# Kernel optimization log

Hardware: AMD Instinct MI355X
Metric: run time of the kernel (lower is better)

## Reference

```python
import jax, jax.numpy as jnp
import numpy as np

N_TOK, BATCH, D, MEM, H, W = 196, 64, 256, 2048, 16, 16


def setup_inputs() -> dict:
    key = jax.random.key(0)
    ks = jax.random.split(key, 9)
    w_scale = 1.0 / np.sqrt(D)  # ~ Linear default init scale
    return {
        "input_tokens": jax.random.normal(ks[0], (N_TOK, BATCH, D), jnp.float32),
        "ch_memory": jax.random.normal(ks[1], (MEM, D), jnp.float32) * 0.1,
        "ch_wq": jax.random.normal(ks[2], (D, D), jnp.float32) * w_scale,
        "ch_wk": jax.random.normal(ks[3], (D, D), jnp.float32) * w_scale,
        "ch_wv": jax.random.normal(ks[4], (D, D), jnp.float32) * w_scale,
        "sp_memory": jax.random.normal(ks[5], (MEM, H, W), jnp.float32) * 0.1,
        "sp_wq": jax.random.normal(ks[6], (D, D), jnp.float32) * w_scale,
        "sp_wk": jax.random.normal(ks[7], (D, D), jnp.float32) * w_scale,
        "sp_wv": jax.random.normal(ks[8], (D, D), jnp.float32) * w_scale,
    }


def reference(input_tokens, ch_memory, ch_wq, ch_wk, ch_wv,
              sp_memory, sp_wq, sp_wk, sp_wv):
    n_tok, batch, d = input_tokens.shape
    hw = d  # spatial branch requires feature_dim == H*W
    x = input_tokens.reshape(n_tok * batch, d)  # [NB, D]

    # ---- Channel memory branch: dot-product softmax read ----
    q = x @ ch_wq.T                       # [NB, D]
    k = ch_memory @ ch_wk.T               # [M, D]
    v = ch_memory @ ch_wv.T               # [M, D]
    scores = (q @ k.T) * (1.0 / jnp.sqrt(jnp.float32(d)))  # [NB, M]
    att_c = jax.nn.softmax(scores, axis=-1)
    out_c = att_c @ v                     # [NB, D]

    # ---- Spatial memory branch: SSIM-score softmax read ----
    mem_flat = sp_memory.reshape(sp_memory.shape[0], hw)  # [M, HW]
    qf = x @ sp_wq.T                      # [NB, HW]
    kf = mem_flat @ sp_wk.T               # [M, HW]
    vf = mem_flat @ sp_wv.T               # [M, HW]

    q_mean = jnp.mean(qf, axis=1, keepdims=True)          # [NB, 1]
    k_mean = jnp.mean(kf, axis=1, keepdims=True)          # [M, 1]
    q_var = jnp.var(qf, axis=1, ddof=1, keepdims=True)    # unbiased, like torch.var
    k_var = jnp.var(kf, axis=1, ddof=1, keepdims=True)
    cov = ((qf - q_mean) @ (kf - k_mean).T) / jnp.float32(hw - 1)  # [NB, M]

    c1, c2 = 0.01, 0.03
    mean_prod = q_mean @ k_mean.T                          # [NB, M]
    numerator = (2.0 * mean_prod + c1) * (2.0 * cov + c2)
    denominator = (q_mean ** 2 + (k_mean.T) ** 2 + c1) * (q_var + k_var.T + c2)
    ssim = numerator / (denominator + 1e-8)                # [NB, M]

    att_s = jax.nn.softmax(ssim, axis=-1)
    out_s = att_s @ vf                     # [NB, HW] == [NB, D]

    return (out_c + out_s).reshape(n_tok, batch, d)
```

## Files before the change

kernel.cpp:

```cpp
#include <hip/hip_runtime.h>

#define NBQ 12544
#define DM  256
#define MM  2048

typedef __attribute__((ext_vector_type(8)))  __bf16 bf16x8;
typedef __attribute__((ext_vector_type(4)))  float  floatx4;

__device__ __forceinline__ ushort f2bf(float x) {
    unsigned u = __float_as_uint(x);
    u += 0x7fffu + ((u >> 16) & 1u);
    return (ushort)(u >> 16);
}
__device__ __forceinline__ float bf2f(ushort h) {
    return __uint_as_float(((unsigned)h) << 16);
}

__global__ __launch_bounds__(256) void gemm_proj_all(
    const float* __restrict__ x,      const float* __restrict__ ch_mem,
    const float* __restrict__ ch_wq,  const float* __restrict__ ch_wk,
    const float* __restrict__ ch_wv,  const float* __restrict__ sp_mem,
    const float* __restrict__ sp_wq,  const float* __restrict__ sp_wk,
    const float* __restrict__ sp_wv,
    ushort* __restrict__ Qb,  ushort* __restrict__ QFb,
    ushort* __restrict__ Kb,  ushort* __restrict__ KFb,
    ushort* __restrict__ Vtb, ushort* __restrict__ VFtb)
{
    __shared__ ushort As[64][72];
    __shared__ ushort Ws[64][72];

    int bid = blockIdx.x;
    const float* A; const float* W; ushort* C; int nrows, trans;
    if (bid < 1568) {
        if (bid < 784) { A = x; W = ch_wq; C = Qb; }
        else           { A = x; W = sp_wq; C = QFb; bid -= 784; }
        nrows = NBQ; trans = 0;
    } else if (bid < 1824) {
        if (bid < 1696) { A = ch_mem; W = ch_wk; C = Kb;  bid -= 1568; }
        else            { A = sp_mem; W = sp_wk; C = KFb; bid -= 1696; }
        nrows = MM; trans = 0;
    } else {
        if (bid < 1952) { A = ch_mem; W = ch_wv; C = Vtb;  bid -= 1824; }
        else            { A = sp_mem; W = sp_wv; C = VFtb; bid -= 1952; }
        nrows = MM; trans = 1;
    }
    const int r0 = (bid >> 2) * 64;
    const int c0 = (bid & 3) * 64;

    const int tid  = threadIdx.x;
    const int wv   = tid >> 6;
    const int lane = tid & 63;
    const int quad = lane >> 4;
    const int l16  = lane & 15;
    const int rw = (wv & 1) * 32;
    const int cw = (wv >> 1) * 32;

    floatx4 acc[2][2];
    #pragma unroll
    for (int i = 0; i < 2; ++i)
        #pragma unroll
        for (int j = 0; j < 2; ++j)
            acc[i][j] = (floatx4){0.f, 0.f, 0.f, 0.f};

    for (int d0 = 0; d0 < 256; d0 += 64) {
        __syncthreads();
        #pragma unroll
        for (int it = 0; it < 4; ++it) {
            int idx = tid + it * 256;
            int r = idx >> 4, c4 = (idx & 15) * 4;
            float4 a4 = *(const float4*)(A + (size_t)(r0 + r) * 256 + d0 + c4);
            float4 w4 = *(const float4*)(W + (size_t)(c0 + r) * 256 + d0 + c4);
            ushort4 ab, wb;
            ab.x = f2bf(a4.x); ab.y = f2bf(a4.y); ab.z = f2bf(a4.z); ab.w = f2bf(a4.w);
            wb.x = f2bf(w4.x); wb.y = f2bf(w4.y); wb.z = f2bf(w4.z); wb.w = f2bf(w4.w);
            *(ushort4*)&As[r][c4] = ab;
            *(ushort4*)&Ws[r][c4] = wb;
        }
        __syncthreads();
        #pragma unroll
        for (int kk = 0; kk < 64; kk += 32) {
            bf16x8 aA0 = *(const bf16x8*)&As[rw + l16][kk + quad * 8];
            bf16x8 aA1 = *(const bf16x8*)&As[rw + 16 + l16][kk + quad * 8];
            bf16x8 bW0 = *(const bf16x8*)&Ws[cw + l16][kk + quad * 8];
            bf16x8 bW1 = *(const bf16x8*)&Ws[cw + 16 + l16][kk + quad * 8];
            acc[0][0] = __builtin_amdgcn_mfma_f32_16x16x32_bf16(aA0, bW0, acc[0][0], 0, 0, 0);
            acc[0][1] = __builtin_amdgcn_mfma_f32_16x16x32_bf16(aA0, bW1, acc[0][1], 0, 0, 0);
            acc[1][0] = __builtin_amdgcn_mfma_f32_16x16x32_bf16(aA1, bW0, acc[1][0], 0, 0, 0);
            acc[1][1] = __builtin_amdgcn_mfma_f32_16x16x32_bf16(aA1, bW1, acc[1][1], 0, 0, 0);
        }
    }

    if (!trans) {
        #pragma unroll
        for (int ag = 0; ag < 2; ++ag)
            #pragma unroll
            for (int cg = 0; cg < 2; ++cg)
                #pragma unroll
                for (int i = 0; i < 4; ++i)
                    C[(size_t)(r0 + rw + ag * 16 + quad * 4 + i) * 256
                      + c0 + cw + cg * 16 + l16] = f2bf(acc[ag][cg][i]);
    } else {
        __syncthreads();
        #pragma unroll
        for (int ag = 0; ag < 2; ++ag)
            #pragma unroll
            for (int cg = 0; cg < 2; ++cg)
                #pragma unroll
                for (int i = 0; i < 4; ++i)
                    Ws[cw + cg * 16 + l16][rw + ag * 16 + quad * 4 + i] = f2bf(acc[ag][cg][i]);
        __syncthreads();
        const int col = tid >> 2;
        const int seg = (tid & 3) * 16;
        #pragma unroll
        for (int j = 0; j < 2; ++j)
            *(uint4*)(C + (size_t)(c0 + col) * nrows + r0 + seg + j * 8) =
                *(const uint4*)&Ws[col][seg + j * 8];
    }
}

__global__ __launch_bounds__(256) void row_stats_all(
    const ushort* __restrict__ QFb, const ushort* __restrict__ KFb,
    float* __restrict__ qm, float* __restrict__ qv,
    float* __restrict__ km, float* __restrict__ kv)
{
    const int rt   = blockIdx.x * 4 + (threadIdx.x >> 6);
    const int lane = threadIdx.x & 63;
    const ushort* X; float* mean; float* var; int row;
    if (rt < NBQ) { X = QFb; mean = qm; var = qv; row = rt; }
    else          { X = KFb; mean = km; var = kv; row = rt - NBQ; }
    ushort4 u = *(const ushort4*)(X + (size_t)row * 256 + lane * 4);
    float a = bf2f(u.x), b = bf2f(u.y), c = bf2f(u.z), d = bf2f(u.w);
    float s  = a + b + c + d;
    float ss = a * a + b * b + c * c + d * d;
    #pragma unroll
    for (int off = 32; off > 0; off >>= 1) {
        s  += __shfl_down(s, off);
        ss += __shfl_down(ss, off);
    }
    if (lane == 0) {
        float m = s * (1.f / 256.f);
        mean[row] = m;
        var[row]  = (ss - 256.f * m * m) * (1.f / 255.f);
    }
}

__global__ __launch_bounds__(256, 2) void fused_attn_mfma(
    const ushort* __restrict__ Qb,  const ushort* __restrict__ QFb,
    const ushort* __restrict__ Kb,  const ushort* __restrict__ KFb,
    const ushort* __restrict__ Vtb, const ushort* __restrict__ VFtb,
    const float* __restrict__ qm_, const float* __restrict__ qv_,
    const float* __restrict__ km_, const float* __restrict__ kv_,
    float* __restrict__ out)
{
    __shared__ ushort K_lds[32][264];
    __shared__ ushort KF_lds[32][264];
    __shared__ ushort Vt_lds[256][40];
    __shared__ ushort VFt_lds[256][40];
    __shared__ ushort P_lds[2][32][36];

    const int tid  = threadIdx.x;
    const int wv   = tid >> 6;
    const int lane = tid & 63;
    const int quad = lane >> 4;
    const int l16  = lane & 15;
    const int qsel = wv & 1;
    const int ksel = wv >> 1;
    const int q0   = blockIdx.x * 32;

    bf16x8 aQ[8], aQF[8];
    {
        const ushort* qp  = Qb  + (size_t)(q0 + qsel * 16 + l16) * DM + quad * 8;
        const ushort* qfp = QFb + (size_t)(q0 + qsel * 16 + l16) * DM + quad * 8;
        #pragma unroll
        for (int s = 0; s < 8; ++s) {
            aQ[s]  = *(const bf16x8*)(qp  + s * 32);
            aQF[s] = *(const bf16x8*)(qfp + s * 32);
        }
    }
    float qmv[4], qvv[4];
    #pragma unroll
    for (int r = 0; r < 4; ++r) {
        int qg = q0 + qsel * 16 + quad * 4 + r;
        qmv[r] = qm_[qg]; qvv[r] = qv_[qg];
    }

    floatx4 acc_c[8], acc_s[8];
    #pragma unroll
    for (int t = 0; t < 8; ++t) {
        acc_c[t] = (floatx4){0.f, 0.f, 0.f, 0.f};
        acc_s[t] = (floatx4){0.f, 0.f, 0.f, 0.f};
    }
    float denc_r[4] = {0.f, 0.f, 0.f, 0.f};
    float dens_r[4] = {0.f, 0.f, 0.f, 0.f};

    for (int kt = 0; kt < MM; kt += 32) {
        __syncthreads();
        #pragma unroll
        for (int it = 0; it < 4; ++it) {
            int idx = tid + it * 256;
            int r = idx >> 5, c8 = (idx & 31) * 8;
            *(uint4*)&K_lds[r][c8]  = *(const uint4*)(Kb  + (size_t)(kt + r) * DM + c8);
            *(uint4*)&KF_lds[r][c8] = *(const uint4*)(KFb + (size_t)(kt + r) * DM + c8);
        }
        #pragma unroll
        for (int it = 0; it < 4; ++it) {
            int idx = tid + it * 256;
            int d = idx >> 2, kc = (idx & 3) * 8;
            *(uint4*)&Vt_lds[d][kc]  = *(const uint4*)(Vtb  + (size_t)d * MM + kt + kc);
            *(uint4*)&VFt_lds[d][kc] = *(const uint4*)(VFtb + (size_t)d * MM + kt + kc);
        }
        __syncthreads();

        floatx4 sc = (floatx4){0.f, 0.f, 0.f, 0.f};
        floatx4 sd = (floatx4){0.f, 0.f, 0.f, 0.f};
        #pragma unroll
        for (int s = 0; s < 8; ++s) {
            bf16x8 bK  = *(const bf16x8*)&K_lds[ksel * 16 + l16][s * 32 + quad * 8];
            bf16x8 bKF = *(const bf16x8*)&KF_lds[ksel * 16 + l16][s * 32 + quad * 8];
            sc = __builtin_amdgcn_mfma_f32_16x16x32_bf16(aQ[s],  bK,  sc, 0, 0, 0);
            sd = __builtin_amdgcn_mfma_f32_16x16x32_bf16(aQF[s], bKF, sd, 0, 0, 0);
        }
        {
            float kmv = km_[kt + ksel * 16 + l16];
            float kvv = kv_[kt + ksel * 16 + l16];
            #pragma unroll
            for (int r = 0; r < 4; ++r) {
                float p1  = __expf(sc[r] * 0.0625f);
                float mp  = qmv[r] * kmv;
                float cov = (sd[r] - 256.f * mp) * (1.f / 255.f);
                float num = (2.f * mp + 0.01f) * (2.f * cov + 0.03f);
                float den = (qmv[r] * qmv[r] + kmv * kmv + 0.01f) * (qvv[r] + kvv + 0.03f);
                float p2  = __expf(num / (den + 1e-8f));
                P_lds[0][qsel * 16 + quad * 4 + r][ksel * 16 + l16] = f2bf(p1);
                P_lds[1][qsel * 16 + quad * 4 + r][ksel * 16 + l16] = f2bf(p2);
                denc_r[r] += p1;
                dens_r[r] += p2;
            }
        }
        __syncthreads();
        bf16x8 aPc = *(const bf16x8*)&P_lds[0][qsel * 16 + l16][quad * 8];
        bf16x8 aPs = *(const bf16x8*)&P_lds[1][qsel * 16 + l16][quad * 8];
        #pragma unroll
        for (int t = 0; t < 8; ++t) {
            int d0 = ksel * 128 + t * 16;
            bf16x8 bV  = *(const bf16x8*)&Vt_lds[d0 + l16][quad * 8];
            bf16x8 bVF = *(const bf16x8*)&VFt_lds[d0 + l16][quad * 8];
            acc_c[t] = __builtin_amdgcn_mfma_f32_16x16x32_bf16(aPc, bV,  acc_c[t], 0, 0, 0);
            acc_s[t] = __builtin_amdgcn_mfma_f32_16x16x32_bf16(aPs, bVF, acc_s[t], 0, 0, 0);
        }
    }

    #pragma unroll
    for (int r = 0; r < 4; ++r) {
        #pragma unroll
        for (int m = 1; m < 16; m <<= 1) {
            denc_r[r] += __shfl_xor(denc_r[r], m, 64);
            dens_r[r] += __shfl_xor(dens_r[r], m, 64);
        }
    }
    __syncthreads();
    float* denbuf = (float*)P_lds;
    if (l16 == 0) {
        #pragma unroll
        for (int r = 0; r < 4; ++r) {
            int q32 = qsel * 16 + quad * 4 + r;
            denbuf[ksel * 32 + q32]      = denc_r[r];
            denbuf[64 + ksel * 32 + q32] = dens_r[r];
        }
    }
    __syncthreads();
    #pragma unroll
    for (int r = 0; r < 4; ++r) {
        int q32 = qsel * 16 + quad * 4 + r;
        float rc = 1.f / (denbuf[q32] + denbuf[32 + q32]);
        float rs = 1.f / (denbuf[64 + q32] + denbuf[96 + q32]);
        float* orow = out + (size_t)(q0 + q32) * DM + ksel * 128 + l16;
        #pragma unroll
        for (int t = 0; t < 8; ++t)
            orow[t * 16] = acc_c[t][r] * rc + acc_s[t][r] * rs;
    }
}

extern "C" void kernel_launch(void* const* d_in, const int* in_sizes, int n_in,
                              void* d_out, int out_size, void* d_ws, size_t ws_size,
                              hipStream_t stream)
{
    const float* x      = (const float*)d_in[0];
    const float* ch_mem = (const float*)d_in[1];
    const float* ch_wq  = (const float*)d_in[2];
    const float* ch_wk  = (const float*)d_in[3];
    const float* ch_wv  = (const float*)d_in[4];
    const float* sp_mem = (const float*)d_in[5];
    const float* sp_wq  = (const float*)d_in[6];
    const float* sp_wk  = (const float*)d_in[7];
    const float* sp_wv  = (const float*)d_in[8];
    float* out = (float*)d_out;

    ushort* Qb   = (ushort*)d_ws;
    ushort* QFb  = Qb   + (size_t)NBQ * DM;
    ushort* Kb   = QFb  + (size_t)NBQ * DM;
    ushort* KFb  = Kb   + (size_t)MM * DM;
    ushort* Vtb  = KFb  + (size_t)MM * DM;
    ushort* VFtb = Vtb  + (size_t)MM * DM;
    float*  qm   = (float*)(VFtb + (size_t)MM * DM);
    float*  qv   = qm + NBQ;
    float*  km   = qv + NBQ;
    float*  kv   = km + MM;

    dim3 blk(256);
    gemm_proj_all<<<dim3(2080), blk, 0, stream>>>(
        x, ch_mem, ch_wq, ch_wk, ch_wv, sp_mem, sp_wq, sp_wk, sp_wv,
        Qb, QFb, Kb, KFb, Vtb, VFtb);
    row_stats_all<<<dim3((NBQ + MM) / 4), blk, 0, stream>>>(QFb, KFb, qm, qv, km, kv);
    fused_attn_mfma<<<dim3(NBQ / 32), blk, 0, stream>>>(
        Qb, QFb, Kb, KFb, Vtb, VFtb, qm, qv, km, kv, out);
}
```

Baseline: 280.2 us.

## Share A tile across paired projections and repack V tiles in LDS

The projection GEMM now computes two outputs that share the same A input (Q and QF from x, K and V from each memory) in one block. Each A tile is loaded and converted to bf16 once instead of twice, and the grid is halved. The attention kernel's V/VF LDS tiles are rearranged to 128 rows of 72 elements, which changes the global-load and LDS-read pattern, likely to reduce bank conflicts. The price is more accumulator registers and LDS in the GEMM, which may lower occupancy.

```diff
diff --git a/kernel.cpp b/kernel.cpp
--- a/kernel.cpp
+++ b/kernel.cpp
@@ -27,22 +27,20 @@
     ushort* __restrict__ Vtb, ushort* __restrict__ VFtb)
 {
     __shared__ ushort As[64][72];
-    __shared__ ushort Ws[64][72];
+    __shared__ ushort W1s[64][72];
+    __shared__ ushort W2s[64][72];
 
     int bid = blockIdx.x;
-    const float* A; const float* W; ushort* C; int nrows, trans;
-    if (bid < 1568) {
-        if (bid < 784) { A = x; W = ch_wq; C = Qb; }
-        else           { A = x; W = sp_wq; C = QFb; bid -= 784; }
-        nrows = NBQ; trans = 0;
-    } else if (bid < 1824) {
-        if (bid < 1696) { A = ch_mem; W = ch_wk; C = Kb;  bid -= 1568; }
-        else            { A = sp_mem; W = sp_wk; C = KFb; bid -= 1696; }
-        nrows = MM; trans = 0;
+    const float* A; const float* W1; const float* W2;
+    ushort* C1; ushort* C2; int nrows, trans2;
+    if (bid < 784) {
+        A = x; W1 = ch_wq; W2 = sp_wq; C1 = Qb; C2 = QFb; nrows = NBQ; trans2 = 0;
+    } else if (bid < 912) {
+        A = ch_mem; W1 = ch_wk; W2 = ch_wv; C1 = Kb; C2 = Vtb;
+        nrows = MM; trans2 = 1; bid -= 784;
     } else {
-        if (bid < 1952) { A = ch_mem; W = ch_wv; C = Vtb;  bid -= 1824; }
-        else            { A = sp_mem; W = sp_wv; C = VFtb; bid -= 1952; }
-        nrows = MM; trans = 1;
+        A = sp_mem; W1 = sp_wk; W2 = sp_wv; C1 = KFb; C2 = VFtb;
+        nrows = MM; trans2 = 1; bid -= 912;
     }
     const int r0 = (bid >> 2) * 64;
     const int c0 = (bid & 3) * 64;
@@ -55,12 +53,14 @@
     const int rw = (wv & 1) * 32;
     const int cw = (wv >> 1) * 32;
 
-    floatx4 acc[2][2];
+    floatx4 acc1[2][2], acc2[2][2];
     #pragma unroll
     for (int i = 0; i < 2; ++i)
         #pragma unroll
-        for (int j = 0; j < 2; ++j)
-            acc[i][j] = (floatx4){0.f, 0.f, 0.f, 0.f};
+        for (int j = 0; j < 2; ++j) {
+            acc1[i][j] = (floatx4){0.f, 0.f, 0.f, 0.f};
+            acc2[i][j] = (floatx4){0.f, 0.f, 0.f, 0.f};
+        }
 
     for (int d0 = 0; d0 < 256; d0 += 64) {
         __syncthreads();
@@ -68,37 +68,55 @@
         for (int it = 0; it < 4; ++it) {
             int idx = tid + it * 256;
             int r = idx >> 4, c4 = (idx & 15) * 4;
-            float4 a4 = *(const float4*)(A + (size_t)(r0 + r) * 256 + d0 + c4);
-            float4 w4 = *(const float4*)(W + (size_t)(c0 + r) * 256 + d0 + c4);
-            ushort4 ab, wb;
-            ab.x = f2bf(a4.x); ab.y = f2bf(a4.y); ab.z = f2bf(a4.z); ab.w = f2bf(a4.w);
-            wb.x = f2bf(w4.x); wb.y = f2bf(w4.y); wb.z = f2bf(w4.z); wb.w = f2bf(w4.w);
-            *(ushort4*)&As[r][c4] = ab;
-            *(ushort4*)&Ws[r][c4] = wb;
+            float4 a4 = *(const float4*)(A  + (size_t)(r0 + r) * 256 + d0 + c4);
+            float4 w14 = *(const float4*)(W1 + (size_t)(c0 + r) * 256 + d0 + c4);
+            float4 w24 = *(const float4*)(W2 + (size_t)(c0 + r) * 256 + d0 + c4);
+            ushort4 ab, w1b, w2b;
+            ab.x = f2bf(a4.x);  ab.y = f2bf(a4.y);  ab.z = f2bf(a4.z);  ab.w = f2bf(a4.w);
+            w1b.x = f2bf(w14.x); w1b.y = f2bf(w14.y); w1b.z = f2bf(w14.z); w1b.w = f2bf(w14.w);
+            w2b.x = f2bf(w24.x); w2b.y = f2bf(w24.y); w2b.z = f2bf(w24.z); w2b.w = f2bf(w24.w);
+            *(ushort4*)&As[r][c4]  = ab;
+            *(ushort4*)&W1s[r][c4] = w1b;
+            *(ushort4*)&W2s[r][c4] = w2b;
         }
         __syncthreads();
         #pragma unroll
         for (int kk = 0; kk < 64; kk += 32) {
             bf16x8 aA0 = *(const bf16x8*)&As[rw + l16][kk + quad * 8];
             bf16x8 aA1 = *(const bf16x8*)&As[rw + 16 + l16][kk + quad * 8];
-            bf16x8 bW0 = *(const bf16x8*)&Ws[cw + l16][kk + quad * 8];
-            bf16x8 bW1 = *(const bf16x8*)&Ws[cw + 16 + l16][kk + quad * 8];
-            acc[0][0] = __builtin_amdgcn_mfma_f32_16x16x32_bf16(aA0, bW0, acc[0][0], 0, 0, 0);
-            acc[0][1] = __builtin_amdgcn_mfma_f32_16x16x32_bf16(aA0, bW1, acc[0][1], 0, 0, 0);
-            acc[1][0] = __builtin_amdgcn_mfma_f32_16x16x32_bf16(aA1, bW0, acc[1][0], 0, 0, 0);
-            acc[1][1] = __builtin_amdgcn_mfma_f32_16x16x32_bf16(aA1, bW1, acc[1][1], 0, 0, 0);
-        }
-    }
-
-    if (!trans) {
+            bf16x8 b10 = *(const bf16x8*)&W1s[cw + l16][kk + quad * 8];
+            bf16x8 b11 = *(const bf16x8*)&W1s[cw + 16 + l16][kk + quad * 8];
+            bf16x8 b20 = *(const bf16x8*)&W2s[cw + l16][kk + quad * 8];
+            bf16x8 b21 = *(const bf16x8*)&W2s[cw + 16 + l16][kk + quad * 8];
+            acc1[0][0] = __builtin_amdgcn_mfma_f32_16x16x32_bf16(aA0, b10, acc1[0][0], 0, 0, 0);
+            acc1[0][1] = __builtin_amdgcn_mfma_f32_16x16x32_bf16(aA0, b11, acc1[0][1], 0, 0, 0);
+            acc1[1][0] = __builtin_amdgcn_mfma_f32_16x16x32_bf16(aA1, b10, acc1[1][0], 0, 0, 0);
+            acc1[1][1] = __builtin_amdgcn_mfma_f32_16x16x32_bf16(aA1, b11, acc1[1][1], 0, 0, 0);
+            acc2[0][0] = __builtin_amdgcn_mfma_f32_16x16x32_bf16(aA0, b20, acc2[0][0], 0, 0, 0);
+            acc2[0][1] = __builtin_amdgcn_mfma_f32_16x16x32_bf16(aA0, b21, acc2[0][1], 0, 0, 0);
+            acc2[1][0] = __builtin_amdgcn_mfma_f32_16x16x32_bf16(aA1, b20, acc2[1][0], 0, 0, 0);
+            acc2[1][1] = __builtin_amdgcn_mfma_f32_16x16x32_bf16(aA1, b21, acc2[1][1], 0, 0, 0);
+        }
+    }
+
+    #pragma unroll
+    for (int ag = 0; ag < 2; ++ag)
+        #pragma unroll
+        for (int cg = 0; cg < 2; ++cg)
+            #pragma unroll
+            for (int i = 0; i < 4; ++i)
+                C1[(size_t)(r0 + rw + ag * 16 + quad * 4 + i) * 256
+                   + c0 + cw + cg * 16 + l16] = f2bf(acc1[ag][cg][i]);
+
+    if (!trans2) {
         #pragma unroll
         for (int ag = 0; ag < 2; ++ag)
             #pragma unroll
             for (int cg = 0; cg < 2; ++cg)
                 #pragma unroll
                 for (int i = 0; i < 4; ++i)
-                    C[(size_t)(r0 + rw + ag * 16 + quad * 4 + i) * 256
-                      + c0 + cw + cg * 16 + l16] = f2bf(acc[ag][cg][i]);
+                    C2[(size_t)(r0 + rw + ag * 16 + quad * 4 + i) * 256
+                       + c0 + cw + cg * 16 + l16] = f2bf(acc2[ag][cg][i]);
     } else {
         __syncthreads();
         #pragma unroll
@@ -107,14 +125,14 @@
             for (int cg = 0; cg < 2; ++cg)
                 #pragma unroll
                 for (int i = 0; i < 4; ++i)
-                    Ws[cw + cg * 16 + l16][rw + ag * 16 + quad * 4 + i] = f2bf(acc[ag][cg][i]);
+                    W2s[cw + cg * 16 + l16][rw + ag * 16 + quad * 4 + i] = f2bf(acc2[ag][cg][i]);
         __syncthreads();
         const int col = tid >> 2;
         const int seg = (tid & 3) * 16;
         #pragma unroll
         for (int j = 0; j < 2; ++j)
-            *(uint4*)(C + (size_t)(c0 + col) * nrows + r0 + seg + j * 8) =
-                *(const uint4*)&Ws[col][seg + j * 8];
+            *(uint4*)(C2 + (size_t)(c0 + col) * nrows + r0 + seg + j * 8) =
+                *(const uint4*)&W2s[col][seg + j * 8];
     }
 }
 
@@ -154,8 +172,8 @@
 {
     __shared__ ushort K_lds[32][264];
     __shared__ ushort KF_lds[32][264];
-    __shared__ ushort Vt_lds[256][40];
-    __shared__ ushort VFt_lds[256][40];
+    __shared__ ushort VV_c[128][72];
+    __shared__ ushort VV_s[128][72];
     __shared__ ushort P_lds[2][32][36];
 
     const int tid  = threadIdx.x;
@@ -205,9 +223,12 @@
         #pragma unroll
         for (int it = 0; it < 4; ++it) {
             int idx = tid + it * 256;
-            int d = idx >> 2, kc = (idx & 3) * 8;
-            *(uint4*)&Vt_lds[d][kc]  = *(const uint4*)(Vtb  + (size_t)d * MM + kt + kc);
-            *(uint4*)&VFt_lds[d][kc] = *(const uint4*)(VFtb + (size_t)d * MM + kt + kc);
+            int r = idx >> 3, c = idx & 7;
+            int dhi = c >> 2, kc = c & 3;
+            int col = dhi * 32 + kc * 8;
+            size_t g = (size_t)(r + dhi * 128) * MM + kt + kc * 8;
+            *(uint4*)&VV_c[r][col] = *(const uint4*)(Vtb  + g);
+            *(uint4*)&VV_s[r][col] = *(const uint4*)(VFtb + g);
         }
         __syncthreads();
 
@@ -242,9 +263,10 @@
         bf16x8 aPs = *(const bf16x8*)&P_lds[1][qsel * 16 + l16][quad * 8];
         #pragma unroll
         for (int t = 0; t < 8; ++t) {
-            int d0 = ksel * 128 + t * 16;
-            bf16x8 bV  = *(const bf16x8*)&Vt_lds[d0 + l16][quad * 8];
-            bf16x8 bVF = *(const bf16x8*)&VFt_lds[d0 + l16][quad * 8];
+            int row = t * 16 + l16;
+            int col = ksel * 32 + quad * 8;
+            bf16x8 bV  = *(const bf16x8*)&VV_c[row][col];
+            bf16x8 bVF = *(const bf16x8*)&VV_s[row][col];
             acc_c[t] = __builtin_amdgcn_mfma_f32_16x16x32_bf16(aPc, bV,  acc_c[t], 0, 0, 0);
             acc_s[t] = __builtin_amdgcn_mfma_f32_16x16x32_bf16(aPs, bVF, acc_s[t], 0, 0, 0);
         }
@@ -308,7 +330,7 @@
     float*  kv   = km + MM;
 
     dim3 blk(256);
-    gemm_proj_all<<<dim3(2080), blk, 0, stream>>>(
+    gemm_proj_all<<<dim3(1040), blk, 0, stream>>>(
         x, ch_mem, ch_wq, ch_wk, ch_wv, sp_mem, sp_wq, sp_wk, sp_wv,
         Qb, QFb, Kb, KFb, Vtb, VFtb);
     row_stats_all<<<dim3((NBQ + MM) / 4), blk, 0, stream>>>(QFb, KFb, qm, qv, km, kv);
```

Measured after the change: 423.6 us. 1.51x slower.
